# Optimization experiments

Measured on AMD Instinct MI355X. Metric: run time of the kernel, lower is better.

## Reference

```python
import jax, jax.numpy as jnp
import numpy as np

TOP_K = 30
NUM_RBF = 16
NUM_POS = 16
MAX_REL = 32
EDGE_FEATURES = 128
EDGE_IN = NUM_POS + NUM_RBF * 9 + 7  # 167


def _normalize(x, axis=-1):
    # torch F.normalize: x / max(||x||, 1e-12)
    return x / jnp.maximum(jnp.linalg.norm(x, axis=axis, keepdims=True), 1e-12)


def _gather_nodes(nodes, idx):
    # nodes [B,L,C], idx [B,L,K] -> [B,L,K,C]
    return jax.vmap(lambda n, i: n[i])(nodes, idx)


def _rbf(D):
    D_mu = jnp.linspace(2.0, 22.0, NUM_RBF)  # [R]
    D_sigma = (22.0 - 2.0) / NUM_RBF
    return jnp.exp(-(((D[..., None] - D_mu) / D_sigma) ** 2))


def _get_rbf(A, B, E_idx):
    # full pairwise dist then gather neighbors (faithful to source)
    D_A_B = jnp.sqrt(jnp.sum((A[:, :, None, :] - B[:, None, :, :]) ** 2, -1) + 1e-6)
    D_nb = jnp.take_along_axis(D_A_B, E_idx, axis=2)  # [B,L,K]
    return _rbf(D_nb)


def _quaternions(R):
    # R [B,L,K,3,3] -> Q [B,L,K,4]
    diag = jnp.diagonal(R, axis1=-2, axis2=-1)  # [B,L,K,3]
    Rxx, Ryy, Rzz = diag[..., 0], diag[..., 1], diag[..., 2]
    magnitudes = 0.5 * jnp.sqrt(jnp.abs(1 + jnp.stack(
        [Rxx - Ryy - Rzz, -Rxx + Ryy - Rzz, -Rxx - Ryy + Rzz], -1)))
    signs = jnp.sign(jnp.stack([
        R[..., 2, 1] - R[..., 1, 2],
        R[..., 0, 2] - R[..., 2, 0],
        R[..., 1, 0] - R[..., 0, 1]], -1))
    xyz = signs * magnitudes
    w = jnp.sqrt(jax.nn.relu(1 + jnp.sum(diag, -1, keepdims=True))) / 2.0
    return _normalize(jnp.concatenate((xyz, w), -1))


def _orientations_coarse(X, E_idx, eps=1e-6):
    B, L, _ = X.shape
    dX = X[:, 1:, :] - X[:, :-1, :]
    dX_norm = jnp.linalg.norm(dX, axis=-1)
    dX_mask = (dX_norm > 3.6) & (dX_norm < 4.0)
    dX = dX * dX_mask[:, :, None]
    U = _normalize(dX)
    u_2, u_1, u_0 = U[:, :-2, :], U[:, 1:-1, :], U[:, 2:, :]
    n_2 = _normalize(jnp.cross(u_2, u_1))
    o_1 = _normalize(u_2 - u_1)
    # local frames O [B,L-3,3,3] -> flattened, padded to [B,L,9]
    O = jnp.stack((o_1, n_2, jnp.cross(o_1, n_2)), 2).reshape(B, L - 3, 9)
    O = jnp.pad(O, ((0, 0), (1, 2), (0, 0)))
    O_neighbors = _gather_nodes(O, E_idx)        # [B,L,K,9]
    X_neighbors = _gather_nodes(X, E_idx)        # [B,L,K,3]
    O = O.reshape(B, L, 3, 3)
    O_neighbors = O_neighbors.reshape(*E_idx.shape, 3, 3)
    dXn = X_neighbors - X[:, :, None, :]
    dU = _normalize(jnp.einsum('blij,blkj->blki', O, dXn))
    R = jnp.einsum('blji,blkjm->blkim', O, O_neighbors)  # O^T @ O_nb
    Q = _quaternions(R)
    return jnp.concatenate((dU, Q), -1)  # [B,L,K,7]


def setup_inputs() -> dict:
    B, L = 2, 4096
    key = jax.random.key(0)
    ks = jax.random.split(key, 6)
    Ca = jax.random.normal(ks[0], (B, L, 3), dtype=jnp.float32)
    mask = jnp.ones((B, L), dtype=jnp.float32)
    residue_idx = jnp.arange(B * L, dtype=jnp.int32).reshape(B, L)
    chain_labels = jnp.sort(jax.random.randint(ks[1], (B, L), 0, 4), axis=-1).astype(jnp.int32)
    pos_in = 2 * MAX_REL + 1 + 1  # 66
    pos_W = jax.random.normal(ks[2], (NUM_POS, pos_in), dtype=jnp.float32) / np.sqrt(pos_in)
    pos_b = jnp.zeros((NUM_POS,), dtype=jnp.float32)
    edge_W = jax.random.normal(ks[3], (EDGE_FEATURES, EDGE_IN), dtype=jnp.float32) / np.sqrt(EDGE_IN)
    ln_g = jnp.ones((EDGE_FEATURES,), dtype=jnp.float32)
    ln_b = jnp.zeros((EDGE_FEATURES,), dtype=jnp.float32)
    return {"Ca": Ca, "mask": mask, "residue_idx": residue_idx,
            "chain_labels": chain_labels, "pos_W": pos_W, "pos_b": pos_b,
            "edge_W": edge_W, "ln_g": ln_g, "ln_b": ln_b}


def _forward(Ca, mask, residue_idx, chain_labels, pos_W, pos_b, edge_W, ln_g, ln_b):
    B, L, _ = Ca.shape
    # _dist: masked pairwise distances + kNN
    mask_2D = mask[:, :, None] * mask[:, None, :]
    dX = Ca[:, None, :, :] - Ca[:, :, None, :]
    D = mask_2D * jnp.sqrt(jnp.sum(dX ** 2, 3) + 1e-6)
    D_max = jnp.max(D, -1, keepdims=True)
    D_adjust = D + (1.0 - mask_2D) * D_max
    k = min(TOP_K, L)
    neg_vals, E_idx = jax.lax.top_k(-D_adjust, k)  # smallest-k
    D_neighbors = -neg_vals

    zeros = jnp.zeros((B, 1, 3), dtype=Ca.dtype)
    Ca_0 = jnp.concatenate([zeros, Ca[:, :-1, :]], axis=1)
    Ca_1 = Ca
    Ca_2 = jnp.concatenate([Ca[:, 1:, :], zeros], axis=1)

    O_features = _orientations_coarse(Ca, E_idx)

    RBF_all = jnp.concatenate([
        _rbf(D_neighbors),
        _get_rbf(Ca_0, Ca_0, E_idx), _get_rbf(Ca_2, Ca_2, E_idx),
        _get_rbf(Ca_0, Ca_1, E_idx), _get_rbf(Ca_0, Ca_2, E_idx),
        _get_rbf(Ca_1, Ca_0, E_idx), _get_rbf(Ca_1, Ca_2, E_idx),
        _get_rbf(Ca_2, Ca_0, E_idx), _get_rbf(Ca_2, Ca_1, E_idx)], axis=-1)

    offset = residue_idx[:, :, None] - residue_idx[:, None, :]
    offset = jnp.take_along_axis(offset, E_idx, axis=2)  # [B,L,K]
    d_chains = (chain_labels[:, :, None] - chain_labels[:, None, :] == 0).astype(jnp.int32)
    E_chains = jnp.take_along_axis(d_chains, E_idx, axis=2)

    # PositionalEncodings
    d = jnp.clip(offset + MAX_REL, 0, 2 * MAX_REL) * E_chains + (1 - E_chains) * (2 * MAX_REL + 1)
    d_onehot = jax.nn.one_hot(d, 2 * MAX_REL + 2, dtype=jnp.float32)
    E_positional = d_onehot @ pos_W.T + pos_b

    E = jnp.concatenate((E_positional, RBF_all, O_features), -1)  # [B,L,K,167]
    E = E @ edge_W.T
    mu = jnp.mean(E, -1, keepdims=True)
    var = jnp.var(E, -1, keepdims=True)
    E = (E - mu) / jnp.sqrt(var + 1e-5) * ln_g + ln_b
    return E, E_idx


def reference(Ca, mask, residue_idx, chain_labels, pos_W, pos_b, edge_W, ln_g, ln_b):
    return _forward(Ca, mask, residue_idx, chain_labels, pos_W, pos_b, edge_W, ln_g, ln_b)
```

## Files before the change

### kernel.cpp

```cpp
#include <hip/hip_runtime.h>
#include <stdint.h>

#define LL 4096
#define NB 2
#define KK 30
#define CDIM 128
#define FROW 200

typedef _Float16 half_t;
typedef half_t half8 __attribute__((ext_vector_type(8)));
typedef float f32x4 __attribute__((ext_vector_type(4)));

__device__ __forceinline__ float3 loadCa(const float* __restrict__ Ca, int b, int idx) {
    const float* p = Ca + ((size_t)(b * LL + idx)) * 3;
    return make_float3(p[0], p[1], p[2]);
}
__device__ __forceinline__ float3 loadCa4(const f32x4* __restrict__ Ca4, int b, int idx) {
    f32x4 v = Ca4[b * LL + idx];
    return make_float3(v[0], v[1], v[2]);
}
__device__ __forceinline__ float3 shiftedCa4(const f32x4* __restrict__ Ca4, int b, int idx, int sel) {
    int jj = idx + sel - 1;
    if (jj < 0 || jj >= LL) return make_float3(0.f, 0.f, 0.f);
    return loadCa4(Ca4, b, jj);
}
__device__ __forceinline__ float sgnf(float x) { return (x > 0.f) ? 1.f : ((x < 0.f) ? -1.f : 0.f); }
__device__ __forceinline__ float pdist(float3 a, float3 c) {
    float dx = a.x - c.x, dy = a.y - c.y, dz = a.z - c.z;
    return sqrtf(dx * dx + dy * dy + dz * dz + 1e-6f);
}

__global__ __launch_bounds__(256) void prep_kernel(const float* __restrict__ W,
                                                   const float* __restrict__ posW,
                                                   const float* __restrict__ posb,
                                                   const float* __restrict__ Ca,
                                                   half_t* __restrict__ Bp,
                                                   half_t* __restrict__ pwt,
                                                   float* __restrict__ Of,
                                                   f32x4* __restrict__ Ca4) {
    int blk = blockIdx.x;
    int tid = threadIdx.x;
    if (blk < 12) {
        int idx = blk * 256 + tid;
        if (idx >= 8 * 6 * 64) return;
        int l = idx & 63;
        int ts = idx >> 6;
        int s = ts % 6, t = ts / 6;
        int n = 16 * t + (l & 15);
        int kbase = 32 * s + 8 * (l >> 4);
        half8 v;
#pragma unroll
        for (int e = 0; e < 8; e++) {
            int k = kbase + e;
            v[e] = (k < 167) ? (half_t)W[n * 167 + k] : (half_t)0.f;
        }
        *(half8*)(Bp + (size_t)idx * 8) = v;
    } else if (blk < 17) {
        int idx = (blk - 12) * 256 + tid;
        if (idx < 66 * 16) {
            int d = idx >> 4, p = idx & 15;
            pwt[d * 16 + p] = (half_t)(posW[p * 66 + d] + posb[p]);
        }
    } else {
        int t = (blk - 17) * 256 + tid;
        if (t >= NB * LL) return;
        int b = t >> 12, i = t & (LL - 1);
        f32x4 c4;
        c4[0] = Ca[(size_t)t * 3];
        c4[1] = Ca[(size_t)t * 3 + 1];
        c4[2] = Ca[(size_t)t * 3 + 2];
        c4[3] = 0.f;
        Ca4[t] = c4;
        float o[9] = {0.f, 0.f, 0.f, 0.f, 0.f, 0.f, 0.f, 0.f, 0.f};
        if (i >= 1 && i <= LL - 3) {
            float3 cm = loadCa(Ca, b, i - 1), cc = loadCa(Ca, b, i), cp = loadCa(Ca, b, i + 1);
            float dx0 = cc.x - cm.x, dy0 = cc.y - cm.y, dz0 = cc.z - cm.z;
            float n0 = sqrtf(dx0 * dx0 + dy0 * dy0 + dz0 * dz0);
            float k0 = (n0 > 3.6f && n0 < 4.0f) ? 1.f : 0.f;
            float s0 = k0 / fmaxf(n0 * k0, 1e-12f);
            float u2x = dx0 * s0, u2y = dy0 * s0, u2z = dz0 * s0;
            float dx1 = cp.x - cc.x, dy1 = cp.y - cc.y, dz1 = cp.z - cc.z;
            float n1 = sqrtf(dx1 * dx1 + dy1 * dy1 + dz1 * dz1);
            float k1 = (n1 > 3.6f && n1 < 4.0f) ? 1.f : 0.f;
            float s1 = k1 / fmaxf(n1 * k1, 1e-12f);
            float u1x = dx1 * s1, u1y = dy1 * s1, u1z = dz1 * s1;
            float cx = u2y * u1z - u2z * u1y;
            float cy = u2z * u1x - u2x * u1z;
            float cz = u2x * u1y - u2y * u1x;
            float cn = sqrtf(cx * cx + cy * cy + cz * cz);
            float cinv = 1.f / fmaxf(cn, 1e-12f);
            float n2x = cx * cinv, n2y = cy * cinv, n2z = cz * cinv;
            float ox = u2x - u1x, oy = u2y - u1y, oz = u2z - u1z;
            float on = sqrtf(ox * ox + oy * oy + oz * oz);
            float oinv = 1.f / fmaxf(on, 1e-12f);
            float o1x = ox * oinv, o1y = oy * oinv, o1z = oz * oinv;
            o[0] = o1x; o[1] = o1y; o[2] = o1z;
            o[3] = n2x; o[4] = n2y; o[5] = n2z;
            o[6] = o1y * n2z - o1z * n2y;
            o[7] = o1z * n2x - o1x * n2z;
            o[8] = o1x * n2y - o1y * n2x;
        }
        float* dst = Of + (size_t)t * 9;
#pragma unroll
        for (int r = 0; r < 9; r++) dst[r] = o[r];
    }
}

__global__ __launch_bounds__(256, 8) void topk_kernel(const f32x4* __restrict__ Ca4,
                                                      const float* __restrict__ mask,
                                                      int* __restrict__ eidx_ws,
                                                      float* __restrict__ dnb_ws,
                                                      float* __restrict__ out_eidx_f) {
    __shared__ unsigned long long cand[512];
    __shared__ int wint[2][4];
    __shared__ int gcnt[4];
    __shared__ float wflt[4];
    int row = blockIdx.x;
    int b = row >> 12;
    int tid = threadIdx.x;
    int w = tid >> 6, lane = tid & 63;
    float3 ci = loadCa4(Ca4, b, row & (LL - 1));
    float mi = mask[row];
    float dreg[16];
    unsigned mfl = 0;
    float localmax = 0.f;
#pragma unroll
    for (int s = 0; s < 16; s++) {
        int j = tid + s * 256;
        f32x4 pj = Ca4[b * LL + j];
        float dx = pj[0] - ci.x, dy = pj[1] - ci.y, dz = pj[2] - ci.z;
        float d = sqrtf(dx * dx + dy * dy + dz * dz + 1e-6f);
        float m2 = mi * mask[b * LL + j];
        float D = m2 * d;
        dreg[s] = D;
        mfl |= (m2 == 0.f ? 1u : 0u) << s;
        localmax = fmaxf(localmax, D);
    }
#pragma unroll
    for (int o = 32; o; o >>= 1) localmax = fmaxf(localmax, __shfl_xor(localmax, o));
    if (lane == 0) wflt[w] = localmax;
    __syncthreads();
    float dmax = fmaxf(fmaxf(wflt[0], wflt[1]), fmaxf(wflt[2], wflt[3]));
    unsigned ui[16];
#pragma unroll
    for (int s = 0; s < 16; s++)
        ui[s] = __float_as_uint(dreg[s] + (((mfl >> s) & 1) ? dmax : 0.f));
    unsigned lo = 0u, hi = 0x7f800000u, T = 0u;
    bool found = false;
    int p = 0;
    for (int it = 0; it < 24 && !found; ++it) {
        unsigned mid = (lo + hi) >> 1;
        int c = 0;
#pragma unroll
        for (int s = 0; s < 16; s++) c += (ui[s] < mid) ? 1 : 0;
#pragma unroll
        for (int o = 32; o; o >>= 1) c += __shfl_xor(c, o);
        if (lane == 0) wint[p][w] = c;
        __syncthreads();
        c = wint[p][0] + wint[p][1] + wint[p][2] + wint[p][3];
        p ^= 1;
        if (c < 30) lo = mid;
        else if (c > 64) hi = mid;
        else { T = mid; found = true; }
    }
    if (!found) T = hi;
    int cnt = 0;
#pragma unroll
    for (int s = 0; s < 16; s++) cnt += (ui[s] < T) ? 1 : 0;
    int inc = cnt;
#pragma unroll
    for (int o = 1; o < 64; o <<= 1) {
        int nv = __shfl_up(inc, o);
        if (lane >= o) inc += nv;
    }
    if (lane == 63) gcnt[w] = inc;
    __syncthreads();
    int C = gcnt[0] + gcnt[1] + gcnt[2] + gcnt[3];
    int waveoff = 0;
    for (int q = 0; q < 4; q++) waveoff += (q < w) ? gcnt[q] : 0;
    int slot = waveoff + inc - cnt;
#pragma unroll
    for (int s = 0; s < 16; s++) {
        if (ui[s] < T) {
            int j = tid + s * 256;
            if (slot < 512)
                cand[slot] = ((unsigned long long)ui[s] << 32) | (unsigned)j;
            slot++;
        }
    }
    __syncthreads();
    if (w != 0) return;
    if (C <= 64) {
        unsigned long long v = (lane < C) ? cand[lane] : ~0ull;
#pragma unroll
        for (int k = 2; k <= 64; k <<= 1) {
#pragma unroll
            for (int jj = k >> 1; jj > 0; jj >>= 1) {
                unsigned long long o = __shfl_xor(v, jj);
                bool take_min = (((lane & jj) == 0) == ((lane & k) == 0));
                bool lt = (o < v);
                v = (take_min == lt) ? o : v;
            }
        }
        if (lane < KK) {
            int j = (int)(v & 0xffffffffu);
            eidx_ws[row * KK + lane] = j;
            dnb_ws[row * KK + lane] = __uint_as_float((unsigned)(v >> 32));
            out_eidx_f[row * KK + lane] = (float)j;
        }
    } else {
        unsigned long long r[8];
#pragma unroll
        for (int q = 0; q < 8; q++) {
            int idx = lane + 64 * q;
            r[q] = (idx < C && idx < 512) ? cand[idx] : ~0ull;
        }
        for (int t = 0; t < KK; t++) {
            unsigned long long v = r[0];
#pragma unroll
            for (int q = 1; q < 8; q++) v = (r[q] < v) ? r[q] : v;
#pragma unroll
            for (int o = 32; o; o >>= 1) {
                unsigned long long u = __shfl_xor(v, o);
                if (u < v) v = u;
            }
            if (lane == 0) {
                int j = (int)(v & 0xffffffffu);
                eidx_ws[row * KK + t] = j;
                dnb_ws[row * KK + t] = __uint_as_float((unsigned)(v >> 32));
                out_eidx_f[row * KK + t] = (float)j;
            }
#pragma unroll
            for (int q = 0; q < 8; q++)
                if (r[q] == v) r[q] = ~0ull;
        }
    }
}

__global__ __launch_bounds__(256) void edge_kernel(const f32x4* __restrict__ Ca4,
                                                   const int* __restrict__ ridx,
                                                   const int* __restrict__ chl,
                                                   const half_t* __restrict__ pwt,
                                                   const half_t* __restrict__ Bp,
                                                   const float* __restrict__ ln_g,
                                                   const float* __restrict__ ln_b,
                                                   const float* __restrict__ Of,
                                                   const int* __restrict__ eidx_ws,
                                                   const float* __restrict__ dnb_ws,
                                                   float* __restrict__ outE) {
    __shared__ alignas(16) half_t featH[64][FROW];
    __shared__ float sD[60][10];
    __shared__ float psum[64][4];
    __shared__ float pssq[64][4];
    __shared__ float rmu[64], rinv[64];
    int row0 = blockIdx.x * 2;
    int b = row0 >> 12;
    int tid = threadIdx.x;

    if (tid < 120) {
        int e = tid >> 1, half = tid & 1;
        int isr1 = (e >= KK) ? 1 : 0;
        int grow = row0 + isr1;
        int ke = e - (isr1 ? KK : 0);
        int i = grow & (LL - 1);
        int j = eidx_ws[grow * KK + ke];
        if (half == 0) {
            float3 Pi0 = shiftedCa4(Ca4, b, i, 0);
            float3 Pi2 = shiftedCa4(Ca4, b, i, 2);
            float3 Pj0 = shiftedCa4(Ca4, b, j, 0);
            float3 Pj1 = loadCa4(Ca4, b, j);
            float3 Pj2 = shiftedCa4(Ca4, b, j, 2);
            sD[e][0] = dnb_ws[grow * KK + ke];
            sD[e][1] = pdist(Pi0, Pj0);
            sD[e][2] = pdist(Pi2, Pj2);
            sD[e][3] = pdist(Pi0, Pj1);
            sD[e][4] = pdist(Pi0, Pj2);
            int off = ridx[grow] - ridx[b * LL + j];
            int eqc = (chl[grow] == chl[b * LL + j]) ? 1 : 0;
            int d = off + 32;
            d = d < 0 ? 0 : (d > 64 ? 64 : d);
            d = eqc ? d : 65;
            *(half8*)&featH[e][0] = *(const half8*)(pwt + d * 16);
            *(half8*)&featH[e][8] = *(const half8*)(pwt + d * 16 + 8);
        } else {
            float3 Pi1 = loadCa4(Ca4, b, i);
            float3 Pi2 = shiftedCa4(Ca4, b, i, 2);
            float3 Pj0 = shiftedCa4(Ca4, b, j, 0);
            float3 Pj1 = loadCa4(Ca4, b, j);
            float3 Pj2 = shiftedCa4(Ca4, b, j, 2);
            sD[e][5] = pdist(Pi1, Pj0);
            sD[e][6] = pdist(Pi1, Pj2);
            sD[e][7] = pdist(Pi2, Pj0);
            sD[e][8] = pdist(Pi2, Pj1);
            float Oi[9], Oj[9];
#pragma unroll
            for (int r = 0; r < 9; r++) {
                Oi[r] = Of[(size_t)grow * 9 + r];
                Oj[r] = Of[((size_t)(b * LL + j)) * 9 + r];
            }
            float dx = Pj1.x - Pi1.x, dy = Pj1.y - Pi1.y, dz = Pj1.z - Pi1.z;
            float v0 = Oi[0] * dx + Oi[1] * dy + Oi[2] * dz;
            float v1 = Oi[3] * dx + Oi[4] * dy + Oi[5] * dz;
            float v2 = Oi[6] * dx + Oi[7] * dy + Oi[8] * dz;
            float nn = sqrtf(v0 * v0 + v1 * v1 + v2 * v2);
            float ninv = 1.f / fmaxf(nn, 1e-12f);
            float R[3][3];
#pragma unroll
            for (int m = 0; m < 3; m++)
#pragma unroll
                for (int n = 0; n < 3; n++)
                    R[m][n] = Oi[0 * 3 + m] * Oj[0 * 3 + n] + Oi[1 * 3 + m] * Oj[1 * 3 + n] +
                              Oi[2 * 3 + m] * Oj[2 * 3 + n];
            float Rxx = R[0][0], Ryy = R[1][1], Rzz = R[2][2];
            float m0 = 0.5f * sqrtf(fabsf(1.f + Rxx - Ryy - Rzz));
            float m1 = 0.5f * sqrtf(fabsf(1.f - Rxx + Ryy - Rzz));
            float m2 = 0.5f * sqrtf(fabsf(1.f - Rxx - Ryy + Rzz));
            float x = sgnf(R[2][1] - R[1][2]) * m0;
            float y = sgnf(R[0][2] - R[2][0]) * m1;
            float z = sgnf(R[1][0] - R[0][1]) * m2;
            float ww = 0.5f * sqrtf(fmaxf(1.f + Rxx + Ryy + Rzz, 0.f));
            float qn = sqrtf(x * x + y * y + z * z + ww * ww);
            float qi = 1.f / fmaxf(qn, 1e-12f);
            half8 h;
            h[0] = (half_t)(v0 * ninv);
            h[1] = (half_t)(v1 * ninv);
            h[2] = (half_t)(v2 * ninv);
            h[3] = (half_t)(x * qi);
            h[4] = (half_t)(y * qi);
            h[5] = (half_t)(z * qi);
            h[6] = (half_t)(ww * qi);
            h[7] = (half_t)0.f;
            half8 zv = {};
            *(half8*)&featH[e][160] = h;
            *(half8*)&featH[e][168] = zv;
            *(half8*)&featH[e][176] = zv;
            *(half8*)&featH[e][184] = zv;
        }
    } else if (tid >= 156) {
        int t = tid - 156;
        int r = 60 + t / 25, c = t % 25;
        half8 zv = {};
        *(half8*)&featH[r][c * 8] = zv;
    }
    __syncthreads();

    for (int job = tid; job < 540; job += 256) {
        int e = job / 9, q = job - e * 9;
        float D = sD[e][q];
        half8 v0, v1;
#pragma unroll
        for (int m = 0; m < 8; m++) {
            float mu = 2.0f + (4.f / 3.f) * (float)m;
            float t = (D - mu) * 0.8f;
            v0[m] = (half_t)exp2f(t * t * -1.4426950408889634f);
        }
#pragma unroll
        for (int m = 8; m < 16; m++) {
            float mu = 2.0f + (4.f / 3.f) * (float)m;
            float t = (D - mu) * 0.8f;
            v1[m - 8] = (half_t)exp2f(t * t * -1.4426950408889634f);
        }
        *(half8*)&featH[e][16 + 16 * q] = v0;
        *(half8*)&featH[e][24 + 16 * q] = v1;
    }
    __syncthreads();

    int lane = tid & 63, w = tid >> 6;
    int cc = lane & 15, g = lane >> 4;
    f32x4 zero = {0.f, 0.f, 0.f, 0.f};
    f32x4 acc[4][2];
#pragma unroll
    for (int m = 0; m < 4; m++) {
        acc[m][0] = zero;
        acc[m][1] = zero;
    }
    const half_t* b0p = Bp + ((size_t)(2 * w) * 6) * 64 * 8;
    const half_t* b1p = Bp + ((size_t)(2 * w + 1) * 6) * 64 * 8;
    for (int s = 0; s < 6; s++) {
        int ko = 32 * s + 8 * g;
        half8 af0 = *(const half8*)&featH[cc][ko];
        half8 af1 = *(const half8*)&featH[16 + cc][ko];
        half8 af2 = *(const half8*)&featH[32 + cc][ko];
        half8 af3 = *(const half8*)&featH[48 + cc][ko];
        half8 bf0 = *(const half8*)(b0p + (size_t)(s * 64 + lane) * 8);
        half8 bf1 = *(const half8*)(b1p + (size_t)(s * 64 + lane) * 8);
        acc[0][0] = __builtin_amdgcn_mfma_f32_16x16x32_f16(af0, bf0, acc[0][0], 0, 0, 0);
        acc[0][1] = __builtin_amdgcn_mfma_f32_16x16x32_f16(af0, bf1, acc[0][1], 0, 0, 0);
        acc[1][0] = __builtin_amdgcn_mfma_f32_16x16x32_f16(af1, bf0, acc[1][0], 0, 0, 0);
        acc[1][1] = __builtin_amdgcn_mfma_f32_16x16x32_f16(af1, bf1, acc[1][1], 0, 0, 0);
        acc[2][0] = __builtin_amdgcn_mfma_f32_16x16x32_f16(af2, bf0, acc[2][0], 0, 0, 0);
        acc[2][1] = __builtin_amdgcn_mfma_f32_16x16x32_f16(af2, bf1, acc[2][1], 0, 0, 0);
        acc[3][0] = __builtin_amdgcn_mfma_f32_16x16x32_f16(af3, bf0, acc[3][0], 0, 0, 0);
        acc[3][1] = __builtin_amdgcn_mfma_f32_16x16x32_f16(af3, bf1, acc[3][1], 0, 0, 0);
    }

#pragma unroll
    for (int m = 0; m < 4; m++) {
#pragma unroll
        for (int q = 0; q < 4; q++) {
            float v0 = acc[m][0][q], v1 = acc[m][1][q];
            float sp = v0 + v1;
            float qp = v0 * v0 + v1 * v1;
#pragma unroll
            for (int o = 1; o < 16; o <<= 1) {
                sp += __shfl_xor(sp, o);
                qp += __shfl_xor(qp, o);
            }
            if (cc == 0) {
                int r = 16 * m + 4 * g + q;
                psum[r][w] = sp;
                pssq[r][w] = qp;
            }
        }
    }
    __syncthreads();
    if (tid < 64) {
        float sum = psum[tid][0] + psum[tid][1] + psum[tid][2] + psum[tid][3];
        float ssq = pssq[tid][0] + pssq[tid][1] + pssq[tid][2] + pssq[tid][3];
        float mu = sum * (1.f / 128.f);
        float var = fmaxf(ssq * (1.f / 128.f) - mu * mu, 0.f);
        rmu[tid] = mu;
        rinv[tid] = 1.f / sqrtf(var + 1e-5f);
    }
    __syncthreads();

    float lgv[2], lbv[2];
#pragma unroll
    for (int tt = 0; tt < 2; tt++) {
        lgv[tt] = ln_g[32 * w + 16 * tt + cc];
        lbv[tt] = ln_b[32 * w + 16 * tt + cc];
    }
#pragma unroll
    for (int m = 0; m < 4; m++) {
#pragma unroll
        for (int q = 0; q < 4; q++) {
            int r = 16 * m + 4 * g + q;
            if (r < 60) {
                float mu = rmu[r], invs = rinv[r];
                int grow = row0 + (r >= KK ? 1 : 0);
                int ke = r - (r >= KK ? KK : 0);
                float* dst = outE + ((size_t)(grow * KK + ke)) * CDIM + 32 * w + cc;
                dst[0] = (acc[m][0][q] - mu) * invs * lgv[0] + lbv[0];
                dst[16] = (acc[m][1][q] - mu) * invs * lgv[1] + lbv[1];
            }
        }
    }
}

extern "C" void kernel_launch(void* const* d_in, const int* in_sizes, int n_in,
                              void* d_out, int out_size, void* d_ws, size_t ws_size,
                              hipStream_t stream) {
    const float* Ca = (const float*)d_in[0];
    const float* mask = (const float*)d_in[1];
    const int* ridx = (const int*)d_in[2];
    const int* chl = (const int*)d_in[3];
    const float* posW = (const float*)d_in[4];
    const float* posb = (const float*)d_in[5];
    const float* edgeW = (const float*)d_in[6];
    const float* lng = (const float*)d_in[7];
    const float* lnb = (const float*)d_in[8];

    float* outE = (float*)d_out;
    float* outEidxF = outE + (size_t)NB * LL * KK * CDIM;

    char* ws = (char*)d_ws;
    half_t* Bp = (half_t*)ws;
    half_t* pwt = (half_t*)(ws + 49152);
    float* Of = (float*)(ws + 51264);
    int* eidx = (int*)(ws + 346176);
    float* dnb = (float*)(ws + 1329216);
    f32x4* Ca4 = (f32x4*)(ws + 2312256);

    prep_kernel<<<17 + (NB * LL + 255) / 256, 256, 0, stream>>>(edgeW, posW, posb, Ca,
                                                                Bp, pwt, Of, Ca4);
    topk_kernel<<<NB * LL, 256, 0, stream>>>(Ca4, mask, eidx, dnb, outEidxF);
    edge_kernel<<<NB * LL / 2, 256, 0, stream>>>(Ca4, ridx, chl, pwt, Bp, lng, lnb,
                                                 Of, eidx, dnb, outE);
}
```

Measured before the change: 120.1 us.

## Process one residue row per edge-kernel block with two waves

The edge kernel now handles one residue (30 edges, padded to 32 rows) per 128-thread block instead of two residues per 256-thread block. Each wave computes 64 output columns over 32 rows rather than 32 columns over 64 rows. This cuts padding waste from 64 to 32 rows per pair of residues and halves shared memory per block, which allows more blocks per CU. In exchange each wave loads twice as many B fragments per row, and there are twice as many blocks, each with its own setup and sync cost.

Result: faster. 115.8 us (-3.6%).

```diff
diff --git a/kernel.cpp b/kernel.cpp
--- a/kernel.cpp
+++ b/kernel.cpp
@@ -237,7 +237,7 @@
     }
 }
 
-__global__ __launch_bounds__(256) void edge_kernel(const f32x4* __restrict__ Ca4,
+__global__ __launch_bounds__(128) void edge_kernel(const f32x4* __restrict__ Ca4,
                                                    const int* __restrict__ ridx,
                                                    const int* __restrict__ chl,
                                                    const half_t* __restrict__ pwt,
@@ -248,29 +248,25 @@
                                                    const int* __restrict__ eidx_ws,
                                                    const float* __restrict__ dnb_ws,
                                                    float* __restrict__ outE) {
-    __shared__ alignas(16) half_t featH[64][FROW];
-    __shared__ float sD[60][10];
-    __shared__ float psum[64][4];
-    __shared__ float pssq[64][4];
-    __shared__ float rmu[64], rinv[64];
-    int row0 = blockIdx.x * 2;
-    int b = row0 >> 12;
+    __shared__ alignas(16) half_t featH[32][FROW];
+    __shared__ float sD[30][10];
+    __shared__ float psum[32][2], pssq[32][2];
+    __shared__ float rmu[32], rinv[32];
+    int grow = blockIdx.x;
+    int b = grow >> 12;
+    int i = grow & (LL - 1);
     int tid = threadIdx.x;
 
-    if (tid < 120) {
+    if (tid < 60) {
         int e = tid >> 1, half = tid & 1;
-        int isr1 = (e >= KK) ? 1 : 0;
-        int grow = row0 + isr1;
-        int ke = e - (isr1 ? KK : 0);
-        int i = grow & (LL - 1);
-        int j = eidx_ws[grow * KK + ke];
+        int j = eidx_ws[grow * KK + e];
         if (half == 0) {
             float3 Pi0 = shiftedCa4(Ca4, b, i, 0);
             float3 Pi2 = shiftedCa4(Ca4, b, i, 2);
             float3 Pj0 = shiftedCa4(Ca4, b, j, 0);
             float3 Pj1 = loadCa4(Ca4, b, j);
             float3 Pj2 = shiftedCa4(Ca4, b, j, 2);
-            sD[e][0] = dnb_ws[grow * KK + ke];
+            sD[e][0] = dnb_ws[grow * KK + e];
             sD[e][1] = pdist(Pi0, Pj0);
             sD[e][2] = pdist(Pi2, Pj2);
             sD[e][3] = pdist(Pi0, Pj1);
@@ -336,15 +332,15 @@
             *(half8*)&featH[e][176] = zv;
             *(half8*)&featH[e][184] = zv;
         }
-    } else if (tid >= 156) {
-        int t = tid - 156;
-        int r = 60 + t / 25, c = t % 25;
+    } else if (tid >= 64 && tid < 114) {
+        int t = tid - 64;
+        int r = 30 + t / 25, c = t % 25;
         half8 zv = {};
         *(half8*)&featH[r][c * 8] = zv;
     }
     __syncthreads();
 
-    for (int job = tid; job < 540; job += 256) {
+    for (int job = tid; job < 270; job += 128) {
         int e = job / 9, q = job - e * 9;
         float D = sD[e][q];
         half8 v0, v1;
@@ -368,39 +364,30 @@
     int lane = tid & 63, w = tid >> 6;
     int cc = lane & 15, g = lane >> 4;
     f32x4 zero = {0.f, 0.f, 0.f, 0.f};
-    f32x4 acc[4][2];
-#pragma unroll
-    for (int m = 0; m < 4; m++) {
-        acc[m][0] = zero;
-        acc[m][1] = zero;
-    }
-    const half_t* b0p = Bp + ((size_t)(2 * w) * 6) * 64 * 8;
-    const half_t* b1p = Bp + ((size_t)(2 * w + 1) * 6) * 64 * 8;
+    f32x4 acc[2][4];
+#pragma unroll
+    for (int m = 0; m < 2; m++)
+#pragma unroll
+        for (int t = 0; t < 4; t++) acc[m][t] = zero;
     for (int s = 0; s < 6; s++) {
         int ko = 32 * s + 8 * g;
         half8 af0 = *(const half8*)&featH[cc][ko];
         half8 af1 = *(const half8*)&featH[16 + cc][ko];
-        half8 af2 = *(const half8*)&featH[32 + cc][ko];
-        half8 af3 = *(const half8*)&featH[48 + cc][ko];
-        half8 bf0 = *(const half8*)(b0p + (size_t)(s * 64 + lane) * 8);
-        half8 bf1 = *(const half8*)(b1p + (size_t)(s * 64 + lane) * 8);
-        acc[0][0] = __builtin_amdgcn_mfma_f32_16x16x32_f16(af0, bf0, acc[0][0], 0, 0, 0);
-        acc[0][1] = __builtin_amdgcn_mfma_f32_16x16x32_f16(af0, bf1, acc[0][1], 0, 0, 0);
-        acc[1][0] = __builtin_amdgcn_mfma_f32_16x16x32_f16(af1, bf0, acc[1][0], 0, 0, 0);
-        acc[1][1] = __builtin_amdgcn_mfma_f32_16x16x32_f16(af1, bf1, acc[1][1], 0, 0, 0);
-        acc[2][0] = __builtin_amdgcn_mfma_f32_16x16x32_f16(af2, bf0, acc[2][0], 0, 0, 0);
-        acc[2][1] = __builtin_amdgcn_mfma_f32_16x16x32_f16(af2, bf1, acc[2][1], 0, 0, 0);
-        acc[3][0] = __builtin_amdgcn_mfma_f32_16x16x32_f16(af3, bf0, acc[3][0], 0, 0, 0);
-        acc[3][1] = __builtin_amdgcn_mfma_f32_16x16x32_f16(af3, bf1, acc[3][1], 0, 0, 0);
-    }
-
-#pragma unroll
-    for (int m = 0; m < 4; m++) {
+#pragma unroll
+        for (int t = 0; t < 4; t++) {
+            half8 bf = *(const half8*)(Bp + ((size_t)(((4 * w + t) * 6 + s) * 64 + lane)) * 8);
+            acc[0][t] = __builtin_amdgcn_mfma_f32_16x16x32_f16(af0, bf, acc[0][t], 0, 0, 0);
+            acc[1][t] = __builtin_amdgcn_mfma_f32_16x16x32_f16(af1, bf, acc[1][t], 0, 0, 0);
+        }
+    }
+
+#pragma unroll
+    for (int m = 0; m < 2; m++) {
 #pragma unroll
         for (int q = 0; q < 4; q++) {
-            float v0 = acc[m][0][q], v1 = acc[m][1][q];
-            float sp = v0 + v1;
-            float qp = v0 * v0 + v1 * v1;
+            float sp = acc[m][0][q] + acc[m][1][q] + acc[m][2][q] + acc[m][3][q];
+            float qp = acc[m][0][q] * acc[m][0][q] + acc[m][1][q] * acc[m][1][q] +
+                       acc[m][2][q] * acc[m][2][q] + acc[m][3][q] * acc[m][3][q];
 #pragma unroll
             for (int o = 1; o < 16; o <<= 1) {
                 sp += __shfl_xor(sp, o);
@@ -414,9 +401,9 @@
         }
     }
     __syncthreads();
-    if (tid < 64) {
-        float sum = psum[tid][0] + psum[tid][1] + psum[tid][2] + psum[tid][3];
-        float ssq = pssq[tid][0] + pssq[tid][1] + pssq[tid][2] + pssq[tid][3];
+    if (tid < 32) {
+        float sum = psum[tid][0] + psum[tid][1];
+        float ssq = pssq[tid][0] + pssq[tid][1];
         float mu = sum * (1.f / 128.f);
         float var = fmaxf(ssq * (1.f / 128.f) - mu * mu, 0.f);
         rmu[tid] = mu;
@@ -424,24 +411,23 @@
     }
     __syncthreads();
 
-    float lgv[2], lbv[2];
-#pragma unroll
-    for (int tt = 0; tt < 2; tt++) {
-        lgv[tt] = ln_g[32 * w + 16 * tt + cc];
-        lbv[tt] = ln_b[32 * w + 16 * tt + cc];
-    }
-#pragma unroll
-    for (int m = 0; m < 4; m++) {
+    float lgv[4], lbv[4];
+#pragma unroll
+    for (int t = 0; t < 4; t++) {
+        lgv[t] = ln_g[64 * w + 16 * t + cc];
+        lbv[t] = ln_b[64 * w + 16 * t + cc];
+    }
+#pragma unroll
+    for (int m = 0; m < 2; m++) {
 #pragma unroll
         for (int q = 0; q < 4; q++) {
             int r = 16 * m + 4 * g + q;
-            if (r < 60) {
+            if (r < KK) {
                 float mu = rmu[r], invs = rinv[r];
-                int grow = row0 + (r >= KK ? 1 : 0);
-                int ke = r - (r >= KK ? KK : 0);
-                float* dst = outE + ((size_t)(grow * KK + ke)) * CDIM + 32 * w + cc;
-                dst[0] = (acc[m][0][q] - mu) * invs * lgv[0] + lbv[0];
-                dst[16] = (acc[m][1][q] - mu) * invs * lgv[1] + lbv[1];
+                float* dst = outE + ((size_t)(grow * KK + r)) * CDIM + 64 * w + cc;
+#pragma unroll
+                for (int t = 0; t < 4; t++)
+                    dst[16 * t] = (acc[m][t][q] - mu) * invs * lgv[t] + lbv[t];
             }
         }
     }
@@ -474,6 +460,6 @@
     prep_kernel<<<17 + (NB * LL + 255) / 256, 256, 0, stream>>>(edgeW, posW, posb, Ca,
                                                                 Bp, pwt, Of, Ca4);
     topk_kernel<<<NB * LL, 256, 0, stream>>>(Ca4, mask, eidx, dnb, outEidxF);
-    edge_kernel<<<NB * LL / 2, 256, 0, stream>>>(Ca4, ridx, chl, pwt, Bp, lng, lnb,
-                                                 Of, eidx, dnb, outE);
-}
+    edge_kernel<<<NB * LL, 128, 0, stream>>>(Ca4, ridx, chl, pwt, Bp, lng, lnb,
+                                             Of, eidx, dnb, outE);
+}
```
